# Kernel tuning notes

Measured on AMD Instinct MI355X. Metric: run time of the kernel, lower is better.

Reference implementation:

```python
import jax, jax.numpy as jnp
import numpy as np

B, T, D = 4, 2048, 1024

def setup_inputs() -> dict:
    key = jax.random.key(0)
    kx, kq, kk, kv = jax.random.split(key, 4)
    lim = 1.0 / np.sqrt(D)
    x = jax.random.normal(kx, (B, T, D), dtype=jnp.float32)
    # nn.Linear weights (stored as [out,in]); applied as x @ W.T
    W_q = jax.random.uniform(kq, (D, D), jnp.float32, -lim, lim)
    W_k = jax.random.uniform(kk, (D, D), jnp.float32, -lim, lim)
    W_v = jax.random.uniform(kv, (D, D), jnp.float32, -lim, lim)
    return {"x": x, "W_q": W_q, "W_k": W_k, "W_v": W_v}

def reference(x, W_q, W_k, W_v):
    d = x.shape[-1]
    Q = jnp.einsum('btd,ed->bte', x, W_q)
    K = jnp.einsum('btd,ed->bte', x, W_k)
    V = jnp.einsum('btd,ed->bte', x, W_v)
    att = jnp.einsum('bqd,bkd->bqk', Q, K) / jnp.sqrt(jnp.asarray(d, x.dtype))
    weights = jax.nn.softmax(att, axis=-1)  # NOTE: original applies no causal mask
    return jnp.einsum('bqk,bkd->bqd', weights, V)
```

## Files before the change

kernel.cpp:

```cpp
#include <hip/hip_runtime.h>
#include <hip/hip_bf16.h>
#include <math.h>
#include <type_traits>


typedef short shortx8 __attribute__((ext_vector_type(8)));
typedef short shortx4 __attribute__((ext_vector_type(4)));
typedef float floatx16 __attribute__((ext_vector_type(16)));
typedef __attribute__((address_space(3))) void lds_void_t;
typedef __attribute__((address_space(1))) const void gmem_void_t;

#define GLD16(gp, lp) \
    __builtin_amdgcn_global_load_lds((gmem_void_t*)(gp), (lds_void_t*)(lp), 16, 0, 0)

#define MODE_PROJ 0
#define MODE_EXP  1
#define MODE_DIV  2

template <int MODE>
__global__ __launch_bounds__(512, 4) void mfma_gemm_abt(
    const __hip_bfloat16* __restrict__ A, const __hip_bfloat16* __restrict__ B,
    void* __restrict__ Cv, float* __restrict__ rowsum,
    __hip_bfloat16* __restrict__ Vt,
    int M, int N, int K, long sA, long sB, long sC, float alpha)
{
    __shared__ __hip_bfloat16 lds[3 * 12288];

    using CT = std::conditional_t<MODE == MODE_DIV, float, __hip_bfloat16>;

    const int z = blockIdx.z;
    A += (long)z * sA;
    B += (long)z * sB;
    CT* C = (CT*)Cv + (long)z * sC;

    const int t     = threadIdx.x;
    const int wave  = t >> 6;
    const int lane  = t & 63;
    const int m0    = blockIdx.x * 256;
    const int n0    = blockIdx.y * 128;
    const int wm    = (wave >> 1) * 64;
    const int wn    = (wave & 1) * 64;
    const int lrow  = lane & 31;
    const int lhalf = lane >> 5;

    const long KU   = (long)(K >> 4);
    const long aOff = (long)((m0 >> 5) + wave) * KU * 512 + lane * 8;
    const long bOff = ((long)((n0 >> 5) + (wave >> 1)) * KU + (wave & 1)) * 512
                      + lane * 8;
    const int  dA   = wave * 1024;
    const int  dB   = 8192 + wave * 512;

    const int raB = (wave >> 1) * 2048 + lane * 8;
    const int rbB = 8192 + (wave & 1) * 2048 + lane * 8;

#define STAGE(bo_, k2_) do {                                               \
        GLD16(A + aOff + (long)(k2_) * 512,       lds + (bo_) + dA);       \
        GLD16(A + aOff + (long)((k2_) + 1) * 512, lds + (bo_) + dA + 512); \
        GLD16(B + bOff + (long)(k2_) * 512,       lds + (bo_) + dB);       \
    } while (0)

    floatx16 acc[2][2] = {};
    const int KT = K >> 5;

    STAGE(0, 0);
    STAGE(12288, 2);

    int rCur = 0;
    int rNxt = 24576;

    for (int kt = 0; kt < KT; ++kt) {
        if (kt == KT - 1) {
            asm volatile("s_waitcnt vmcnt(0)" ::: "memory");
        } else {
            asm volatile("s_waitcnt vmcnt(3)" ::: "memory");
        }
        __builtin_amdgcn_s_barrier();
        if (kt + 2 < KT)
            STAGE(rNxt, 2 * (kt + 2));

        const __hip_bfloat16* Ls = lds + rCur;

        #pragma unroll
        for (int s = 0; s < 2; ++s) {
            shortx8 a[2], b[2];
            #pragma unroll
            for (int i = 0; i < 2; ++i)
                a[i] = *(const shortx8*)(Ls + raB + (2 * i + s) * 512);
            #pragma unroll
            for (int j = 0; j < 2; ++j)
                b[j] = *(const shortx8*)(Ls + rbB + (2 * j + s) * 512);
            __builtin_amdgcn_s_setprio(1);
            #pragma unroll
            for (int i = 0; i < 2; ++i)
                #pragma unroll
                for (int j = 0; j < 2; ++j)
                    acc[i][j] = __builtin_amdgcn_mfma_f32_32x32x16_bf16(
                        a[i], b[j], acc[i][j], 0, 0, 0);
            __builtin_amdgcn_s_setprio(0);
        }
        rCur = (rCur == 24576) ? 0 : rCur + 12288;
        rNxt = (rNxt == 24576) ? 0 : rNxt + 12288;
    }
#undef STAGE

    auto sidx = [&](int row, int col) -> long {
        return ((long)(row >> 5) * (N >> 4) + (col >> 4)) * 512
             + ((row & 31) + 32 * ((col >> 3) & 1)) * 8 + (col & 7);
    };

    if constexpr (MODE == MODE_PROJ) {
        if (z == 2) {
            const int bz   = m0 >> 11;
            const long bo  = (long)bz * N * 2048;
            #pragma unroll
            for (int i = 0; i < 2; ++i)
                #pragma unroll
                for (int j = 0; j < 2; ++j)
                    #pragma unroll
                    for (int g = 0; g < 4; ++g) {
                        const int t0 = (m0 + wm + 32 * i + g * 8 + 4 * lhalf) & 2047;
                        const int d  = n0 + wn + 32 * j + lrow;
                        shortx4 pk;
                        #pragma unroll
                        for (int r = 0; r < 4; ++r) {
                            __hip_bfloat16 hb = __float2bfloat16(acc[i][j][4 * g + r]);
                            pk[r] = *(short*)&hb;
                        }
                        const long idx = bo
                            + ((long)(d >> 5) * 128 + (t0 >> 4)) * 512
                            + ((d & 31) + 32 * ((t0 >> 3) & 1)) * 8 + (t0 & 7);
                        *(shortx4*)(Vt + idx) = pk;
                    }
        } else {
            #pragma unroll
            for (int i = 0; i < 2; ++i)
                #pragma unroll
                for (int j = 0; j < 2; ++j)
                    #pragma unroll
                    for (int g = 0; g < 4; ++g)
                        #pragma unroll
                        for (int r = 0; r < 4; ++r) {
                            const int row = m0 + wm + 32 * i + g * 8 + 4 * lhalf + r;
                            const int col = n0 + wn + 32 * j + lrow;
                            C[sidx(row, col)] = __float2bfloat16(acc[i][j][4 * g + r]);
                        }
        }
    } else if constexpr (MODE == MODE_EXP) {
        #pragma unroll
        for (int i = 0; i < 2; ++i) {
            float rs[16];
            #pragma unroll
            for (int reg = 0; reg < 16; ++reg) rs[reg] = 0.0f;
            #pragma unroll
            for (int j = 0; j < 2; ++j)
                #pragma unroll
                for (int g = 0; g < 4; ++g)
                    #pragma unroll
                    for (int r = 0; r < 4; ++r) {
                        const int row = m0 + wm + 32 * i + g * 8 + 4 * lhalf + r;
                        const int col = n0 + wn + 32 * j + lrow;
                        const float e = __expf(acc[i][j][4 * g + r] * alpha);
                        rs[4 * g + r] += e;
                        C[sidx(row, col)] = __float2bfloat16(e);
                    }
            #pragma unroll
            for (int reg = 0; reg < 16; ++reg) {
                float v = rs[reg];
                v += __shfl_xor(v, 1);
                v += __shfl_xor(v, 2);
                v += __shfl_xor(v, 4);
                v += __shfl_xor(v, 8);
                v += __shfl_xor(v, 16);
                if (lrow == 0) {
                    const long row = m0 + wm + 32 * i + (reg >> 2) * 8 + 4 * lhalf + (reg & 3);
                    atomicAdd(&rowsum[(long)z * M + row], v);
                }
            }
        }
    } else {
        #pragma unroll
        for (int i = 0; i < 2; ++i) {
            float inv[16];
            #pragma unroll
            for (int g = 0; g < 4; ++g)
                #pragma unroll
                for (int r = 0; r < 4; ++r) {
                    const long row = m0 + wm + 32 * i + g * 8 + 4 * lhalf + r;
                    inv[4 * g + r] = 1.0f / rowsum[(long)z * M + row];
                }
            #pragma unroll
            for (int j = 0; j < 2; ++j)
                #pragma unroll
                for (int g = 0; g < 4; ++g)
                    #pragma unroll
                    for (int r = 0; r < 4; ++r) {
                        const long row = m0 + wm + 32 * i + g * 8 + 4 * lhalf + r;
                        const long col = n0 + wn + 32 * j + lrow;
                        C[row * N + col] = acc[i][j][4 * g + r] * inv[4 * g + r];
                    }
        }
    }
}

__global__ __launch_bounds__(256) void prep(
    const float* __restrict__ x,
    const float* __restrict__ W0, const float* __restrict__ W1,
    const float* __restrict__ W2,
    __hip_bfloat16* __restrict__ xb, __hip_bfloat16* __restrict__ Wb,
    float* __restrict__ rowsum)
{
    __shared__ __hip_bfloat16 sb[32768];

    const int b  = blockIdx.x;
    const int tt = threadIdx.x;

    if (b < 32) {
        float4 zz; zz.x = zz.y = zz.z = zz.w = 0.0f;
        ((float4*)rowsum)[b * 256 + tt] = zz;
    }

    const float* src;
    __hip_bfloat16* dst;
    if (b < 256) {
        src = x + (long)b * 32 * 1024;
        dst = xb + (long)b * 32768;
    } else {
        const int w  = (b - 256) >> 5;
        const int rg = (b - 256) & 31;
        src = ((w == 0) ? W0 : (w == 1) ? W1 : W2) + (long)rg * 32 * 1024;
        dst = Wb + (long)w * 1048576 + (long)rg * 32768;
    }

    #pragma unroll
    for (int it = 0; it < 32; ++it) {
        const int idx4 = it * 256 + tt;
        const float4 f = ((const float4*)src)[idx4];
        const int row = idx4 >> 8;
        const int k0  = (idx4 & 255) << 2;
        const int p   = ((row & 31) + 32 * ((k0 >> 3) & 1)) * 8 + (k0 & 7);
        shortx4 pk;
        __hip_bfloat16 h0 = __float2bfloat16(f.x); pk[0] = *(short*)&h0;
        __hip_bfloat16 h1 = __float2bfloat16(f.y); pk[1] = *(short*)&h1;
        __hip_bfloat16 h2 = __float2bfloat16(f.z); pk[2] = *(short*)&h2;
        __hip_bfloat16 h3 = __float2bfloat16(f.w); pk[3] = *(short*)&h3;
        *(shortx4*)(sb + (k0 >> 4) * 512 + p) = pk;
    }
    __syncthreads();

    #pragma unroll
    for (int ot = 0; ot < 16; ++ot) {
        const int off = ot * 2048 + tt * 8;
        *(shortx8*)(dst + off) = *(const shortx8*)(sb + off);
    }
}

extern "C" void kernel_launch(void* const* d_in, const int* in_sizes, int n_in,
                              void* d_out, int out_size, void* d_ws, size_t ws_size,
                              hipStream_t stream)
{
    constexpr int  Bb = 4, T = 2048, D = 1024;
    constexpr int  M  = Bb * T;
    constexpr long TD = (long)T * D;
    constexpr long TT = (long)T * T;
    constexpr long MD = (long)M * D;

    const float* x  = (const float*)d_in[0];
    const float* Wq = (const float*)d_in[1];
    const float* Wk = (const float*)d_in[2];
    const float* Wv = (const float*)d_in[3];
    float* out = (float*)d_out;

    __hip_bfloat16* Q  = (__hip_bfloat16*)d_ws;
    __hip_bfloat16* Kb = Q + MD;
    __hip_bfloat16* Vt = Kb + MD;
    __hip_bfloat16* P  = Vt + MD;
    __hip_bfloat16* xb = P + (long)Bb * TT;
    __hip_bfloat16* Wb = xb + MD;
    float*     rowsum  = (float*)(Wb + 3L * D * D);

    prep<<<dim3(352), dim3(256), 0, stream>>>(x, Wq, Wk, Wv, xb, Wb, rowsum);

    dim3 blk(512);

    mfma_gemm_abt<MODE_PROJ><<<dim3(M / 256, D / 128, 3), blk, 0, stream>>>(
        xb, Wb, Q, nullptr, Vt, M, D, D, 0, (long)D * D, MD, 1.0f);

    mfma_gemm_abt<MODE_EXP><<<dim3(T / 256, T / 128, Bb), blk, 0, stream>>>(
        Q, Kb, P, rowsum, nullptr, T, T, D, TD, TD, TT, 0.03125f);

    mfma_gemm_abt<MODE_DIV><<<dim3(T / 256, D / 128, Bb), blk, 0, stream>>>(
        P, Vt, out, rowsum, nullptr, T, D, T, TT, TD, TD, 1.0f);

    (void)in_sizes; (void)n_in; (void)out_size; (void)ws_size;
}
```

Before: 245.6 us.

## Enlarge GEMM tiles to 256x256 with 64-deep K steps and double buffering

Templates the bf16 MFMA GEMM on tile width so the projection and QK^T launches use 256x256 tiles, with each wave computing a 128x64 block, while the PV launch keeps 128-wide tiles. The K step per iteration doubles to 64. The triple-buffered LDS ring becomes a double buffer, and the next tiles' global-to-LDS loads are interleaved across the four MFMA sub-steps, with extra barriers between them. The aim is higher data reuse per LDS load and fewer grid blocks, in exchange for more registers and LDS per block, a lower occupancy bound (launch_bounds 2), and more synchronisation.

```diff
diff --git a/kernel.cpp b/kernel.cpp
--- a/kernel.cpp
+++ b/kernel.cpp
@@ -17,14 +17,16 @@
 #define MODE_EXP  1
 #define MODE_DIV  2
 
-template <int MODE>
-__global__ __launch_bounds__(512, 4) void mfma_gemm_abt(
+template <int MODE, int BN>
+__global__ __launch_bounds__(512, 2) void mfma_gemm_abt(
     const __hip_bfloat16* __restrict__ A, const __hip_bfloat16* __restrict__ B,
     void* __restrict__ Cv, float* __restrict__ rowsum,
     __hip_bfloat16* __restrict__ Vt,
     int M, int N, int K, long sA, long sB, long sC, float alpha)
 {
-    __shared__ __hip_bfloat16 lds[3 * 12288];
+    constexpr int MI  = (BN == 256) ? 4 : 2;
+    constexpr int BUF = 16384 + (BN == 256 ? 16384 : 8192);
+    __shared__ __hip_bfloat16 lds[2 * BUF];
 
     using CT = std::conditional_t<MODE == MODE_DIV, float, __hip_bfloat16>;
 
@@ -37,71 +39,85 @@
     const int wave  = t >> 6;
     const int lane  = t & 63;
     const int m0    = blockIdx.x * 256;
-    const int n0    = blockIdx.y * 128;
-    const int wm    = (wave >> 1) * 64;
-    const int wn    = (wave & 1) * 64;
+    const int n0    = blockIdx.y * BN;
+    const int wm    = (BN == 256) ? (wave >> 2) * 128 : (wave >> 1) * 64;
+    const int wn    = (BN == 256) ? (wave & 3) * 64   : (wave & 1) * 64;
     const int lrow  = lane & 31;
     const int lhalf = lane >> 5;
 
     const long KU   = (long)(K >> 4);
-    const long aOff = (long)((m0 >> 5) + wave) * KU * 512 + lane * 8;
-    const long bOff = ((long)((n0 >> 5) + (wave >> 1)) * KU + (wave & 1)) * 512
-                      + lane * 8;
-    const int  dA   = wave * 1024;
-    const int  dB   = 8192 + wave * 512;
-
-    const int raB = (wave >> 1) * 2048 + lane * 8;
-    const int rbB = 8192 + (wave & 1) * 2048 + lane * 8;
-
-#define STAGE(bo_, k2_) do {                                               \
-        GLD16(A + aOff + (long)(k2_) * 512,       lds + (bo_) + dA);       \
-        GLD16(A + aOff + (long)((k2_) + 1) * 512, lds + (bo_) + dA + 512); \
-        GLD16(B + bOff + (long)(k2_) * 512,       lds + (bo_) + dB);       \
+    const long aSrc = (long)((m0 >> 5) + wave) * KU * 512 + lane * 8;
+    const long bSrc = (long)((n0 >> 5) + wave) * KU * 512 + lane * 8;
+    const int  dA   = wave * 2048;
+    const int  dB   = 16384 + wave * 2048;
+
+    const int raB = ((BN == 256) ? (wave >> 2) * 8192 : (wave >> 1) * 4096)
+                    + lane * 8;
+    const int rbB = 16384
+                    + ((BN == 256) ? (wave & 3) * 4096 : (wave & 1) * 4096)
+                    + lane * 8;
+
+#define STAGE_Q(bo_, tau_, q_) do {                                            \
+        GLD16(A + aSrc + (long)(4 * (tau_) + (q_)) * 512,                      \
+              lds + (bo_) + dA + (q_) * 512);                                  \
+        if (BN == 256 || wave < 4)                                             \
+            GLD16(B + bSrc + (long)(4 * (tau_) + (q_)) * 512,                  \
+                  lds + (bo_) + dB + (q_) * 512);                              \
     } while (0)
 
-    floatx16 acc[2][2] = {};
-    const int KT = K >> 5;
-
-    STAGE(0, 0);
-    STAGE(12288, 2);
-
-    int rCur = 0;
-    int rNxt = 24576;
+    floatx16 acc[MI][2] = {};
+    const int KT = K >> 6;
+
+    #pragma unroll
+    for (int q = 0; q < 4; ++q) STAGE_Q(0, 0, q);
+    #pragma unroll
+    for (int q = 0; q < 3; ++q) STAGE_Q(BUF, 1, q);
 
     for (int kt = 0; kt < KT; ++kt) {
-        if (kt == KT - 1) {
+        const int bo = (kt & 1) ? BUF : 0;
+        const int bn = bo ^ BUF;
+        if (kt + 1 < KT) {
+            if (BN == 256 || wave < 4)
+                asm volatile("s_waitcnt vmcnt(6)" ::: "memory");
+            else
+                asm volatile("s_waitcnt vmcnt(3)" ::: "memory");
+        } else {
             asm volatile("s_waitcnt vmcnt(0)" ::: "memory");
-        } else {
-            asm volatile("s_waitcnt vmcnt(3)" ::: "memory");
         }
         __builtin_amdgcn_s_barrier();
-        if (kt + 2 < KT)
-            STAGE(rNxt, 2 * (kt + 2));
-
-        const __hip_bfloat16* Ls = lds + rCur;
+        __builtin_amdgcn_sched_barrier(0);
+
+        const __hip_bfloat16* Ls = lds + bo;
 
         #pragma unroll
-        for (int s = 0; s < 2; ++s) {
-            shortx8 a[2], b[2];
-            #pragma unroll
-            for (int i = 0; i < 2; ++i)
-                a[i] = *(const shortx8*)(Ls + raB + (2 * i + s) * 512);
+        for (int s = 0; s < 4; ++s) {
+            shortx8 a[MI], b[2];
+            #pragma unroll
+            for (int i = 0; i < MI; ++i)
+                a[i] = *(const shortx8*)(Ls + raB + i * 2048 + s * 512);
             #pragma unroll
             for (int j = 0; j < 2; ++j)
-                b[j] = *(const shortx8*)(Ls + rbB + (2 * j + s) * 512);
+                b[j] = *(const shortx8*)(Ls + rbB + j * 2048 + s * 512);
+            if (s == 0) {
+                if (kt + 1 < KT) STAGE_Q(bn, kt + 1, 3);
+            } else {
+                if (kt + 2 < KT) STAGE_Q(bo, kt + 2, s - 1);
+            }
+            __builtin_amdgcn_sched_barrier(0);
+            __builtin_amdgcn_s_barrier();
+            __builtin_amdgcn_sched_barrier(0);
             __builtin_amdgcn_s_setprio(1);
             #pragma unroll
-            for (int i = 0; i < 2; ++i)
+            for (int i = 0; i < MI; ++i)
                 #pragma unroll
                 for (int j = 0; j < 2; ++j)
                     acc[i][j] = __builtin_amdgcn_mfma_f32_32x32x16_bf16(
                         a[i], b[j], acc[i][j], 0, 0, 0);
             __builtin_amdgcn_s_setprio(0);
-        }
-        rCur = (rCur == 24576) ? 0 : rCur + 12288;
-        rNxt = (rNxt == 24576) ? 0 : rNxt + 12288;
-    }
-#undef STAGE
+            __builtin_amdgcn_s_barrier();
+        }
+    }
+#undef STAGE_Q
 
     auto sidx = [&](int row, int col) -> long {
         return ((long)(row >> 5) * (N >> 4) + (col >> 4)) * 512
@@ -111,9 +127,9 @@
     if constexpr (MODE == MODE_PROJ) {
         if (z == 2) {
             const int bz   = m0 >> 11;
-            const long bo  = (long)bz * N * 2048;
-            #pragma unroll
-            for (int i = 0; i < 2; ++i)
+            const long bo2 = (long)bz * N * 2048;
+            #pragma unroll
+            for (int i = 0; i < MI; ++i)
                 #pragma unroll
                 for (int j = 0; j < 2; ++j)
                     #pragma unroll
@@ -126,14 +142,14 @@
                             __hip_bfloat16 hb = __float2bfloat16(acc[i][j][4 * g + r]);
                             pk[r] = *(short*)&hb;
                         }
-                        const long idx = bo
+                        const long idx = bo2
                             + ((long)(d >> 5) * 128 + (t0 >> 4)) * 512
                             + ((d & 31) + 32 * ((t0 >> 3) & 1)) * 8 + (t0 & 7);
                         *(shortx4*)(Vt + idx) = pk;
                     }
         } else {
             #pragma unroll
-            for (int i = 0; i < 2; ++i)
+            for (int i = 0; i < MI; ++i)
                 #pragma unroll
                 for (int j = 0; j < 2; ++j)
                     #pragma unroll
@@ -147,7 +163,7 @@
         }
     } else if constexpr (MODE == MODE_EXP) {
         #pragma unroll
-        for (int i = 0; i < 2; ++i) {
+        for (int i = 0; i < MI; ++i) {
             float rs[16];
             #pragma unroll
             for (int reg = 0; reg < 16; ++reg) rs[reg] = 0.0f;
@@ -179,7 +195,7 @@
         }
     } else {
         #pragma unroll
-        for (int i = 0; i < 2; ++i) {
+        for (int i = 0; i < MI; ++i) {
             float inv[16];
             #pragma unroll
             for (int g = 0; g < 4; ++g)
@@ -282,13 +298,13 @@
 
     dim3 blk(512);
 
-    mfma_gemm_abt<MODE_PROJ><<<dim3(M / 256, D / 128, 3), blk, 0, stream>>>(
+    mfma_gemm_abt<MODE_PROJ, 256><<<dim3(M / 256, D / 256, 3), blk, 0, stream>>>(
         xb, Wb, Q, nullptr, Vt, M, D, D, 0, (long)D * D, MD, 1.0f);
 
-    mfma_gemm_abt<MODE_EXP><<<dim3(T / 256, T / 128, Bb), blk, 0, stream>>>(
+    mfma_gemm_abt<MODE_EXP, 256><<<dim3(T / 256, T / 256, Bb), blk, 0, stream>>>(
         Q, Kb, P, rowsum, nullptr, T, T, D, TD, TD, TT, 0.03125f);
 
-    mfma_gemm_abt<MODE_DIV><<<dim3(T / 256, D / 128, Bb), blk, 0, stream>>>(
+    mfma_gemm_abt<MODE_DIV, 128><<<dim3(T / 256, D / 128, Bb), blk, 0, stream>>>(
         P, Vt, out, rowsum, nullptr, T, D, T, TT, TD, TD, 1.0f);
 
     (void)in_sizes; (void)n_in; (void)out_size; (void)ws_size;
```

New measurement: 251.3 us. +2.3%, slower.

## Use 4-wave blocks with 128x64 warp tiles and double-buffered LDS

Applied to the files above, without the earlier changes.

Cuts the block from 8 to 4 waves, so each wave computes a 128x64 output tile (4x2 MFMA tiles) instead of 64x64, giving more register-level reuse of B fragments. The pipeline drops from triple to double buffering, with a full vmcnt(0) wait and a barrier after each k-step. The goal is higher MFMA density per LDS read and a smaller LDS footprint. The cost is fewer waves to hide latency, a shallower prefetch depth and more accumulator registers.

```diff
diff --git a/kernel.cpp b/kernel.cpp
--- a/kernel.cpp
+++ b/kernel.cpp
@@ -18,13 +18,13 @@
 #define MODE_DIV  2
 
 template <int MODE>
-__global__ __launch_bounds__(512, 4) void mfma_gemm_abt(
+__global__ __launch_bounds__(256, 2) void mfma_gemm_abt(
     const __hip_bfloat16* __restrict__ A, const __hip_bfloat16* __restrict__ B,
     void* __restrict__ Cv, float* __restrict__ rowsum,
     __hip_bfloat16* __restrict__ Vt,
     int M, int N, int K, long sA, long sB, long sC, float alpha)
 {
-    __shared__ __hip_bfloat16 lds[3 * 12288];
+    __shared__ __hip_bfloat16 lds[2 * 12288];
 
     using CT = std::conditional_t<MODE == MODE_DIV, float, __hip_bfloat16>;
 
@@ -38,68 +38,65 @@
     const int lane  = t & 63;
     const int m0    = blockIdx.x * 256;
     const int n0    = blockIdx.y * 128;
-    const int wm    = (wave >> 1) * 64;
+    const int wm    = (wave >> 1) * 128;
     const int wn    = (wave & 1) * 64;
     const int lrow  = lane & 31;
     const int lhalf = lane >> 5;
 
     const long KU   = (long)(K >> 4);
-    const long aOff = (long)((m0 >> 5) + wave) * KU * 512 + lane * 8;
-    const long bOff = ((long)((n0 >> 5) + (wave >> 1)) * KU + (wave & 1)) * 512
-                      + lane * 8;
-    const int  dA   = wave * 1024;
-    const int  dB   = 8192 + wave * 512;
-
-    const int raB = (wave >> 1) * 2048 + lane * 8;
+    const long aSrc = (long)((m0 >> 5) + 2 * wave) * KU * 512 + lane * 8;
+    const long bSrc = (long)((n0 >> 5) + wave) * KU * 512 + lane * 8;
+    const int  dA   = wave * 2048;
+    const int  dB   = 8192 + wave * 1024;
+
+    const int raB = (wave >> 1) * 4096 + lane * 8;
     const int rbB = 8192 + (wave & 1) * 2048 + lane * 8;
 
-#define STAGE(bo_, k2_) do {                                               \
-        GLD16(A + aOff + (long)(k2_) * 512,       lds + (bo_) + dA);       \
-        GLD16(A + aOff + (long)((k2_) + 1) * 512, lds + (bo_) + dA + 512); \
-        GLD16(B + bOff + (long)(k2_) * 512,       lds + (bo_) + dB);       \
+#define STAGE(bo_, kt_) do {                                                  \
+        _Pragma("unroll")                                                     \
+        for (int q = 0; q < 2; ++q) {                                         \
+            GLD16(A + aSrc + (long)(2 * (kt_) + q) * 512,                     \
+                  lds + (bo_) + dA + q * 512);                                \
+            GLD16(A + aSrc + (KU + 2 * (kt_) + q) * 512,                      \
+                  lds + (bo_) + dA + 1024 + q * 512);                         \
+            GLD16(B + bSrc + (long)(2 * (kt_) + q) * 512,                     \
+                  lds + (bo_) + dB + q * 512);                                \
+        }                                                                     \
     } while (0)
 
-    floatx16 acc[2][2] = {};
+    floatx16 acc[4][2] = {};
     const int KT = K >> 5;
 
     STAGE(0, 0);
-    STAGE(12288, 2);
-
-    int rCur = 0;
-    int rNxt = 24576;
+    asm volatile("s_waitcnt vmcnt(0)" ::: "memory");
+    __builtin_amdgcn_s_barrier();
 
     for (int kt = 0; kt < KT; ++kt) {
-        if (kt == KT - 1) {
-            asm volatile("s_waitcnt vmcnt(0)" ::: "memory");
-        } else {
-            asm volatile("s_waitcnt vmcnt(3)" ::: "memory");
-        }
-        __builtin_amdgcn_s_barrier();
-        if (kt + 2 < KT)
-            STAGE(rNxt, 2 * (kt + 2));
-
-        const __hip_bfloat16* Ls = lds + rCur;
+        if (kt + 1 < KT)
+            STAGE(((kt + 1) & 1) * 12288, kt + 1);
+
+        const __hip_bfloat16* Ls = lds + (kt & 1) * 12288;
 
         #pragma unroll
         for (int s = 0; s < 2; ++s) {
-            shortx8 a[2], b[2];
-            #pragma unroll
-            for (int i = 0; i < 2; ++i)
-                a[i] = *(const shortx8*)(Ls + raB + (2 * i + s) * 512);
+            shortx8 a[4], b[2];
+            #pragma unroll
+            for (int i = 0; i < 4; ++i)
+                a[i] = *(const shortx8*)(Ls + raB + i * 1024 + s * 512);
             #pragma unroll
             for (int j = 0; j < 2; ++j)
-                b[j] = *(const shortx8*)(Ls + rbB + (2 * j + s) * 512);
+                b[j] = *(const shortx8*)(Ls + rbB + j * 1024 + s * 512);
             __builtin_amdgcn_s_setprio(1);
             #pragma unroll
-            for (int i = 0; i < 2; ++i)
+            for (int i = 0; i < 4; ++i)
                 #pragma unroll
                 for (int j = 0; j < 2; ++j)
                     acc[i][j] = __builtin_amdgcn_mfma_f32_32x32x16_bf16(
                         a[i], b[j], acc[i][j], 0, 0, 0);
             __builtin_amdgcn_s_setprio(0);
         }
-        rCur = (rCur == 24576) ? 0 : rCur + 12288;
-        rNxt = (rNxt == 24576) ? 0 : rNxt + 12288;
+        asm volatile("s_waitcnt vmcnt(0)" ::: "memory");
+        __builtin_amdgcn_s_barrier();
     }
 #undef STAGE
 
@@ -111,9 +108,9 @@
     if constexpr (MODE == MODE_PROJ) {
         if (z == 2) {
             const int bz   = m0 >> 11;
-            const long bo  = (long)bz * N * 2048;
-            #pragma unroll
-            for (int i = 0; i < 2; ++i)
+            const long bo2 = (long)bz * N * 2048;
+            #pragma unroll
+            for (int i = 0; i < 4; ++i)
                 #pragma unroll
                 for (int j = 0; j < 2; ++j)
                     #pragma unroll
@@ -126,14 +123,14 @@
                             __hip_bfloat16 hb = __float2bfloat16(acc[i][j][4 * g + r]);
                             pk[r] = *(short*)&hb;
                         }
-                        const long idx = bo
+                        const long idx = bo2
                             + ((long)(d >> 5) * 128 + (t0 >> 4)) * 512
                             + ((d & 31) + 32 * ((t0 >> 3) & 1)) * 8 + (t0 & 7);
                         *(shortx4*)(Vt + idx) = pk;
                     }
         } else {
             #pragma unroll
-            for (int i = 0; i < 2; ++i)
+            for (int i = 0; i < 4; ++i)
                 #pragma unroll
                 for (int j = 0; j < 2; ++j)
                     #pragma unroll
@@ -147,7 +144,7 @@
         }
     } else if constexpr (MODE == MODE_EXP) {
         #pragma unroll
-        for (int i = 0; i < 2; ++i) {
+        for (int i = 0; i < 4; ++i) {
             float rs[16];
             #pragma unroll
             for (int reg = 0; reg < 16; ++reg) rs[reg] = 0.0f;
@@ -179,7 +176,7 @@
         }
     } else {
         #pragma unroll
-        for (int i = 0; i < 2; ++i) {
+        for (int i = 0; i < 4; ++i) {
             float inv[16];
             #pragma unroll
             for (int g = 0; g < 4; ++g)
@@ -280,7 +277,7 @@
 
     prep<<<dim3(352), dim3(256), 0, stream>>>(x, Wq, Wk, Wv, xb, Wb, rowsum);
 
-    dim3 blk(512);
+    dim3 blk(256);
 
     mfma_gemm_abt<MODE_PROJ><<<dim3(M / 256, D / 128, 3), blk, 0, stream>>>(
         xb, Wb, Q, nullptr, Vt, M, D, D, 0, (long)D * D, MD, 1.0f);
```

Result: no change. 249.9 us (+1.7%).

## Replace LDS-staged GEMM pipeline with direct register loads and smaller tiles

Applied to the files above, without the earlier changes.

Drops the triple-buffered LDS staging through global_load_lds and barriers. Each wave now loads its pre-swizzled A/B fragments straight from global memory into registers with a two-step software prefetch. Block tiles shrink from 256x128 with 512 threads to 128x128 with 256 threads, doubling the grid. This removes LDS traffic and block-wide syncs, but loses data sharing between waves, so each operand fragment is fetched more times from L2/HBM.

```diff
diff --git a/kernel.cpp b/kernel.cpp
--- a/kernel.cpp
+++ b/kernel.cpp
@@ -7,25 +7,18 @@
 typedef short shortx8 __attribute__((ext_vector_type(8)));
 typedef short shortx4 __attribute__((ext_vector_type(4)));
 typedef float floatx16 __attribute__((ext_vector_type(16)));
-typedef __attribute__((address_space(3))) void lds_void_t;
-typedef __attribute__((address_space(1))) const void gmem_void_t;
-
-#define GLD16(gp, lp) \
-    __builtin_amdgcn_global_load_lds((gmem_void_t*)(gp), (lds_void_t*)(lp), 16, 0, 0)
 
 #define MODE_PROJ 0
 #define MODE_EXP  1
 #define MODE_DIV  2
 
 template <int MODE>
-__global__ __launch_bounds__(512, 4) void mfma_gemm_abt(
+__global__ __launch_bounds__(256, 4) void mfma_gemm_abt(
     const __hip_bfloat16* __restrict__ A, const __hip_bfloat16* __restrict__ B,
     void* __restrict__ Cv, float* __restrict__ rowsum,
     __hip_bfloat16* __restrict__ Vt,
     int M, int N, int K, long sA, long sB, long sC, float alpha)
 {
-    __shared__ __hip_bfloat16 lds[3 * 12288];
-
     using CT = std::conditional_t<MODE == MODE_DIV, float, __hip_bfloat16>;
 
     const int z = blockIdx.z;
@@ -36,72 +29,61 @@
     const int t     = threadIdx.x;
     const int wave  = t >> 6;
     const int lane  = t & 63;
-    const int m0    = blockIdx.x * 256;
+    const int m0    = blockIdx.x * 128;
     const int n0    = blockIdx.y * 128;
     const int wm    = (wave >> 1) * 64;
     const int wn    = (wave & 1) * 64;
     const int lrow  = lane & 31;
     const int lhalf = lane >> 5;
 
-    const long KU   = (long)(K >> 4);
-    const long aOff = (long)((m0 >> 5) + wave) * KU * 512 + lane * 8;
-    const long bOff = ((long)((n0 >> 5) + (wave >> 1)) * KU + (wave & 1)) * 512
-                      + lane * 8;
-    const int  dA   = wave * 1024;
-    const int  dB   = 8192 + wave * 512;
-
-    const int raB = (wave >> 1) * 2048 + lane * 8;
-    const int rbB = 8192 + (wave & 1) * 2048 + lane * 8;
-
-#define STAGE(bo_, k2_) do {                                               \
-        GLD16(A + aOff + (long)(k2_) * 512,       lds + (bo_) + dA);       \
-        GLD16(A + aOff + (long)((k2_) + 1) * 512, lds + (bo_) + dA + 512); \
-        GLD16(B + bOff + (long)(k2_) * 512,       lds + (bo_) + dB);       \
-    } while (0)
+    const long KU = (long)(K >> 4);
+    const __hip_bfloat16* pA0 =
+        A + (long)((m0 >> 5) + (wave >> 1) * 2 + 0) * KU * 512 + lane * 8;
+    const __hip_bfloat16* pA1 =
+        A + (long)((m0 >> 5) + (wave >> 1) * 2 + 1) * KU * 512 + lane * 8;
+    const __hip_bfloat16* pB0 =
+        B + (long)((n0 >> 5) + (wave & 1) * 2 + 0) * KU * 512 + lane * 8;
+    const __hip_bfloat16* pB1 =
+        B + (long)((n0 >> 5) + (wave & 1) * 2 + 1) * KU * 512 + lane * 8;
 
     floatx16 acc[2][2] = {};
-    const int KT = K >> 5;
-
-    STAGE(0, 0);
-    STAGE(12288, 2);
-
-    int rCur = 0;
-    int rNxt = 24576;
-
-    for (int kt = 0; kt < KT; ++kt) {
-        if (kt == KT - 1) {
-            asm volatile("s_waitcnt vmcnt(0)" ::: "memory");
-        } else {
-            asm volatile("s_waitcnt vmcnt(3)" ::: "memory");
-        }
-        __builtin_amdgcn_s_barrier();
-        if (kt + 2 < KT)
-            STAGE(rNxt, 2 * (kt + 2));
-
-        const __hip_bfloat16* Ls = lds + rCur;
-
-        #pragma unroll
-        for (int s = 0; s < 2; ++s) {
-            shortx8 a[2], b[2];
-            #pragma unroll
-            for (int i = 0; i < 2; ++i)
-                a[i] = *(const shortx8*)(Ls + raB + (2 * i + s) * 512);
-            #pragma unroll
-            for (int j = 0; j < 2; ++j)
-                b[j] = *(const shortx8*)(Ls + rbB + (2 * j + s) * 512);
-            __builtin_amdgcn_s_setprio(1);
-            #pragma unroll
-            for (int i = 0; i < 2; ++i)
-                #pragma unroll
-                for (int j = 0; j < 2; ++j)
-                    acc[i][j] = __builtin_amdgcn_mfma_f32_32x32x16_bf16(
-                        a[i], b[j], acc[i][j], 0, 0, 0);
-            __builtin_amdgcn_s_setprio(0);
-        }
-        rCur = (rCur == 24576) ? 0 : rCur + 12288;
-        rNxt = (rNxt == 24576) ? 0 : rNxt + 12288;
-    }
-#undef STAGE
+    const int KUi = K >> 4;
+
+    shortx8 x0a, x0b, y0a, y0b;
+    shortx8 x1a, x1b, y1a, y1b;
+
+    x0a = *(const shortx8*)(pA0);
+    x0b = *(const shortx8*)(pA1);
+    y0a = *(const shortx8*)(pB0);
+    y0b = *(const shortx8*)(pB1);
+
+    for (int ku = 0; ku < KUi; ku += 2) {
+        x1a = *(const shortx8*)(pA0 + (long)(ku + 1) * 512);
+        x1b = *(const shortx8*)(pA1 + (long)(ku + 1) * 512);
+        y1a = *(const shortx8*)(pB0 + (long)(ku + 1) * 512);
+        y1b = *(const shortx8*)(pB1 + (long)(ku + 1) * 512);
+
+        __builtin_amdgcn_s_setprio(1);
+        acc[0][0] = __builtin_amdgcn_mfma_f32_32x32x16_bf16(x0a, y0a, acc[0][0], 0, 0, 0);
+        acc[0][1] = __builtin_amdgcn_mfma_f32_32x32x16_bf16(x0a, y0b, acc[0][1], 0, 0, 0);
+        acc[1][0] = __builtin_amdgcn_mfma_f32_32x32x16_bf16(x0b, y0a, acc[1][0], 0, 0, 0);
+        acc[1][1] = __builtin_amdgcn_mfma_f32_32x32x16_bf16(x0b, y0b, acc[1][1], 0, 0, 0);
+        __builtin_amdgcn_s_setprio(0);
+
+        if (ku + 2 < KUi) {
+            x0a = *(const shortx8*)(pA0 + (long)(ku + 2) * 512);
+            x0b = *(const shortx8*)(pA1 + (long)(ku + 2) * 512);
+            y0a = *(const shortx8*)(pB0 + (long)(ku + 2) * 512);
+            y0b = *(const shortx8*)(pB1 + (long)(ku + 2) * 512);
+        }
+
+        __builtin_amdgcn_s_setprio(1);
+        acc[0][0] = __builtin_amdgcn_mfma_f32_32x32x16_bf16(x1a, y1a, acc[0][0], 0, 0, 0);
+        acc[0][1] = __builtin_amdgcn_mfma_f32_32x32x16_bf16(x1a, y1b, acc[0][1], 0, 0, 0);
+        acc[1][0] = __builtin_amdgcn_mfma_f32_32x32x16_bf16(x1b, y1a, acc[1][0], 0, 0, 0);
+        acc[1][1] = __builtin_amdgcn_mfma_f32_32x32x16_bf16(x1b, y1b, acc[1][1], 0, 0, 0);
+        __builtin_amdgcn_s_setprio(0);
+    }
 
     auto sidx = [&](int row, int col) -> long {
         return ((long)(row >> 5) * (N >> 4) + (col >> 4)) * 512
@@ -111,7 +93,7 @@
     if constexpr (MODE == MODE_PROJ) {
         if (z == 2) {
             const int bz   = m0 >> 11;
-            const long bo  = (long)bz * N * 2048;
+            const long bo2 = (long)bz * N * 2048;
             #pragma unroll
             for (int i = 0; i < 2; ++i)
                 #pragma unroll
@@ -126,7 +108,7 @@
                             __hip_bfloat16 hb = __float2bfloat16(acc[i][j][4 * g + r]);
                             pk[r] = *(short*)&hb;
                         }
-                        const long idx = bo
+                        const long idx = bo2
                             + ((long)(d >> 5) * 128 + (t0 >> 4)) * 512
                             + ((d & 31) + 32 * ((t0 >> 3) & 1)) * 8 + (t0 & 7);
                         *(shortx4*)(Vt + idx) = pk;
@@ -280,15 +262,15 @@
 
     prep<<<dim3(352), dim3(256), 0, stream>>>(x, Wq, Wk, Wv, xb, Wb, rowsum);
 
-    dim3 blk(512);
-
-    mfma_gemm_abt<MODE_PROJ><<<dim3(M / 256, D / 128, 3), blk, 0, stream>>>(
+    dim3 blk(256);
+
+    mfma_gemm_abt<MODE_PROJ><<<dim3(M / 128, D / 128, 3), blk, 0, stream>>>(
         xb, Wb, Q, nullptr, Vt, M, D, D, 0, (long)D * D, MD, 1.0f);
 
-    mfma_gemm_abt<MODE_EXP><<<dim3(T / 256, T / 128, Bb), blk, 0, stream>>>(
+    mfma_gemm_abt<MODE_EXP><<<dim3(T / 128, T / 128, Bb), blk, 0, stream>>>(
         Q, Kb, P, rowsum, nullptr, T, T, D, TD, TD, TT, 0.03125f);
 
-    mfma_gemm_abt<MODE_DIV><<<dim3(T / 256, D / 128, Bb), blk, 0, stream>>>(
+    mfma_gemm_abt<MODE_DIV><<<dim3(T / 128, D / 128, Bb), blk, 0, stream>>>(
         P, Vt, out, rowsum, nullptr, T, D, T, TT, TD, TD, 1.0f);
 
     (void)in_sizes; (void)n_in; (void)out_size; (void)ws_size;
```

After: 267.6 us. 1.09x slower.
